# Performance work log

Measured on AMD Instinct MI355X. Metric: run time of the kernel, lower is better.

The kernel has to match this reference:

```python
import jax, jax.numpy as jnp
import numpy as np

K = 49        # k_neighbors
EPS = 1e-5    # BatchNorm2d eps


def setup_inputs() -> dict:
    key = jax.random.key(0)
    ks = jax.random.split(key, 2)
    B, C, M, O = 64, 64, 32, 128
    X = jax.random.normal(ks[0], (B, C, M, M), dtype=jnp.float32)
    # conv1x1 weight (kaiming fan_out) flattened to (O, C); bias init 0
    W = jax.random.normal(ks[1], (O, C), dtype=jnp.float32) * (2.0 / O) ** 0.5
    b = jnp.zeros((O,), jnp.float32)
    gamma = jnp.ones((O,), jnp.float32)
    beta = jnp.zeros((O,), jnp.float32)
    run_mean = jnp.zeros((O,), jnp.float32)
    run_var = jnp.ones((O,), jnp.float32)
    return dict(X=X, W=W, b=b, gamma=gamma, beta=beta,
                run_mean=run_mean, run_var=run_var)


def _knn_aggregate(x):
    """x: (N, C) node features -> D^{-1/2} A D^{-1/2} x for the kNN graph."""
    N = x.shape[0]
    sq = jnp.sum(x * x, axis=1)
    d2 = sq[:, None] + sq[None, :] - 2.0 * (x @ x.T)
    dist = jnp.sqrt(jnp.maximum(d2, 0.0))              # torch.cdist (p=2)
    i = jnp.arange(N)
    dist = dist.at[i, i].set(jnp.inf)                  # fill_diagonal_(inf)
    _, knn = jax.lax.top_k(-dist, K)                   # (N, K) nearest indices
    # topk indices are distinct -> every row degree == K, and the column
    # normalizer uses the col node's row degree (also K), so
    # D^{-1/2} A D^{-1/2} x == mean of gathered neighbors.
    nb = x[knn]                                        # (N, K, C) gather
    return nb.sum(axis=1) / K


def reference(X, W, b, gamma, beta, run_mean, run_var):
    B, C, M, _ = X.shape
    N = M * M
    x = X.reshape(B, C, N).transpose(0, 2, 1)          # (B, N, C) nodes
    Z = jax.vmap(_knn_aggregate)(x)                    # (B, N, C) sparse GCN agg
    # 1x1 conv over the (M, M) grid == per-node linear map
    Fg = jnp.einsum('oc,bnc->bon', W, Z) + b[None, :, None]   # (B, O, N)
    Fg = jax.nn.relu(Fg)
    # BatchNorm2d with running stats (eval mode); Dropout2d is identity in eval
    inv = jax.lax.rsqrt(run_var + EPS)
    Fg = gamma[None, :, None] * (Fg - run_mean[None, :, None]) * inv[None, :, None] + beta[None, :, None]
    return Fg.mean(axis=2)                             # AdaptiveAvgPool2d(1) -> (B, O)
```

## Files before the change

### kernel.cpp

```cpp
#include <hip/hip_runtime.h>
#include <stdint.h>

#define BATCH 64
#define CDIM  64
#define NPTS  1024
#define ODIM  128
#define KNN   49
#define KNNP  52
#define BNEPS 1e-5f
#define ZPAD  72

typedef __attribute__((ext_vector_type(8))) short bf16x8;
typedef __attribute__((ext_vector_type(4))) float f32x4;
typedef union { bf16x8 v; uint32_t d[4]; } bfu;

__device__ __forceinline__ int mbcnt64(unsigned long long m) {
    return __builtin_amdgcn_mbcnt_hi((uint32_t)(m >> 32),
           __builtin_amdgcn_mbcnt_lo((uint32_t)m, 0));
}

__device__ __forceinline__ void bf16_split(float x, uint32_t& h, uint32_t& l) {
    uint32_t u = __float_as_uint(x);
    h = (u + 0x7FFFu + ((u >> 16) & 1u)) >> 16;
    float hf = __uint_as_float(h << 16);
    uint32_t ul = __float_as_uint(x - hf);
    l = (ul + 0x7FFFu + ((ul >> 16) & 1u)) >> 16;
}

#define O_XF   0
#define SZ_XF  (BATCH*64*2*64*8*4)
#define O_SQ   (O_XF + SZ_XF)
#define SZ_SQ  (BATCH*NPTS*4)
#define O_KNN  (O_SQ + SZ_SQ)
#define SZ_KNN (BATCH*NPTS*KNNP*4)
#define O_XFT  (O_KNN + SZ_KNN)
#define SZ_XFT (BATCH*32*4*64*8*4)
#define WS_NEED ((size_t)(O_XFT + SZ_XFT))

__global__ void gcn_init(const float* __restrict__ gamma, const float* __restrict__ beta,
                         const float* __restrict__ rmean, const float* __restrict__ rvar,
                         float* __restrict__ out) {
    int i = blockIdx.x * 256 + threadIdx.x;
    if (i < BATCH * ODIM) {
        int o = i & (ODIM - 1);
        out[i] = beta[o] - gamma[o] * rmean[o] * rsqrtf(rvar[o] + BNEPS);
    }
}

__global__ __launch_bounds__(256) void k0_split(const float* __restrict__ X,
                                                uint32_t* __restrict__ XF,
                                                float* __restrict__ sq,
                                                uint32_t* __restrict__ XFT,
                                                const float* __restrict__ gamma,
                                                const float* __restrict__ beta,
                                                const float* __restrict__ rmean,
                                                const float* __restrict__ rvar,
                                                float* __restrict__ out) {
    if (blockIdx.x < 32) {
        int i = blockIdx.x * 256 + threadIdx.x;
        int o = i & (ODIM - 1);
        out[i] = beta[o] - gamma[o] * rmean[o] * rsqrtf(rvar[o] + BNEPS);
    }
    const int b    = blockIdx.x >> 4;
    const int g    = blockIdx.x & 15;
    const int wv   = threadIdx.x >> 6;
    const int t16  = g * 4 + wv;
    const int lane = threadIdx.x & 63;
    const int n    = t16 * 16 + (lane & 15);
    const int cg   = lane >> 4;
    const float* Xb = X + (size_t)b * CDIM * NPTS;
    float s = 0.f;
    for (int ks = 0; ks < 2; ks++) {
        uint32_t hi[4], lo[4];
#pragma unroll
        for (int dj = 0; dj < 4; dj++) {
            uint32_t hw[2], lw[2];
#pragma unroll
            for (int e = 0; e < 2; e++) {
                int c = ks * 32 + cg * 8 + dj * 2 + e;
                float x = Xb[(size_t)c * NPTS + n];
                s += x * x;
                bf16_split(x, hw[e], lw[e]);
            }
            hi[dj] = hw[0] | (hw[1] << 16);
            lo[dj] = lw[0] | (lw[1] << 16);
        }
        size_t entry = ((size_t)(b * 64 + t16) * 2 + ks) * 64 + lane;
        uint32_t* p = XF + entry * 8;
        *(uint4*)p       = make_uint4(hi[0], hi[1], hi[2], hi[3]);
        *(uint4*)(p + 4) = make_uint4(lo[0], lo[1], lo[2], lo[3]);
    }
    s += __shfl_xor(s, 16, 64);
    s += __shfl_xor(s, 32, 64);
    if (lane < 16) sq[b * NPTS + n] = s;

#pragma unroll
    for (int sx = 0; sx < 2; sx++) {
        int task = g * 8 + wv * 2 + sx;
        int kt = task >> 2, ct = task & 3;
        int c  = ct * 16 + (lane & 15);
        int n0 = kt * 32 + (lane >> 4) * 8;
        const float* xp = Xb + (size_t)c * NPTS + n0;
        uint32_t h[8], l[8];
#pragma unroll
        for (int j = 0; j < 8; j++) bf16_split(xp[j], h[j], l[j]);
        uint32_t* pp = XFT + ((((size_t)b * 32 + kt) * 4 + ct) * 64 + lane) * 8;
        *(uint4*)pp       = make_uint4(h[0] | (h[1] << 16), h[2] | (h[3] << 16),
                                       h[4] | (h[5] << 16), h[6] | (h[7] << 16));
        *(uint4*)(pp + 4) = make_uint4(l[0] | (l[1] << 16), l[2] | (l[3] << 16),
                                       l[4] | (l[5] << 16), l[6] | (l[7] << 16));
    }
}

__global__ __launch_bounds__(512, 6) void k1_gram_select(const uint32_t* __restrict__ XF,
                                                         const float* __restrict__ sq,
                                                         int* __restrict__ knn) {
    __shared__ uint32_t s_pk[8 * 1024];
    const int b    = blockIdx.x >> 6;
    const int rt   = blockIdx.x & 63;
    const int wave = threadIdx.x >> 6, lane = threadIdx.x & 63;
    const int q = lane >> 4, l15 = lane & 15;

    bf16x8 ahi[2], alo[2];
#pragma unroll
    for (int ks = 0; ks < 2; ks++) {
        const uint32_t* p = XF + (((size_t)(b * 64 + rt) * 2 + ks) * 64 + lane) * 8;
        ahi[ks] = *(const bf16x8*)p;
        alo[ks] = *(const bf16x8*)(p + 4);
    }
    const float* sqb = sq + b * NPTS;

#pragma unroll
    for (int tt = 0; tt < 8; tt++) {
        const int t16 = wave * 8 + tt;
        f32x4 acc = {0.f, 0.f, 0.f, 0.f};
#pragma unroll
        for (int ks = 0; ks < 2; ks++) {
            const uint32_t* p = XF + (((size_t)(b * 64 + t16) * 2 + ks) * 64 + lane) * 8;
            bf16x8 bhi = *(const bf16x8*)p;
            bf16x8 blo = *(const bf16x8*)(p + 4);
            acc = __builtin_amdgcn_mfma_f32_16x16x32_bf16(ahi[ks], bhi, acc, 0, 0, 0);
            acc = __builtin_amdgcn_mfma_f32_16x16x32_bf16(alo[ks], bhi, acc, 0, 0, 0);
            acc = __builtin_amdgcn_mfma_f32_16x16x32_bf16(ahi[ks], blo, acc, 0, 0, 0);
        }
        const int col  = t16 * 16 + l15;
        const float sqv = sqb[col];
        uint32_t k16[4];
#pragma unroll
        for (int i = 0; i < 4; i++) {
            int row = q * 4 + i;
            float d = fmaf(-2.f, acc[i], sqv);
            if (col == rt * 16 + row) d = __uint_as_float(0x7F800000u);
            uint32_t u = __float_as_uint(d);
            uint32_t key = ((int)u < 0) ? ~u : (u | 0x80000000u);
            k16[i] = key >> 16;
        }
        const int p0 = 2 * q, p1 = 2 * q + 1;
        s_pk[p0 * 1024 + (col ^ ((p0 & 3) << 3))] = k16[0] | (k16[1] << 16);
        s_pk[p1 * 1024 + (col ^ ((p1 & 3) << 3))] = k16[2] | (k16[3] << 16);
    }
    __syncthreads();

    uint32_t k0r[16], k1r[16];
    {
        const int sw = (wave & 3) << 3;
#pragma unroll
        for (int tt = 0; tt < 16; tt++) {
            uint32_t pk = s_pk[wave * 1024 + ((tt * 64 + lane) ^ sw)];
            k0r[tt] = pk & 0xFFFFu;
            k1r[tt] = pk >> 16;
        }
    }

    uint32_t lo0, hi0, lo1, hi1;
    {
        uint32_t lm0 = k0r[0], lm1 = k1r[0];
#pragma unroll
        for (int tt = 1; tt < 16; tt++) {
            lm0 = k0r[tt] < lm0 ? k0r[tt] : lm0;
            lm1 = k1r[tt] < lm1 ? k1r[tt] : lm1;
        }
        uint32_t g0 = lm0, m0 = lm0, g1 = lm1, m1 = lm1;
#pragma unroll
        for (int off = 1; off < 64; off <<= 1) {
            uint32_t a0 = (uint32_t)__shfl_xor((int)g0, off, 64);
            uint32_t b0 = (uint32_t)__shfl_xor((int)m0, off, 64);
            uint32_t a1 = (uint32_t)__shfl_xor((int)g1, off, 64);
            uint32_t b1 = (uint32_t)__shfl_xor((int)m1, off, 64);
            g0 = a0 < g0 ? a0 : g0;  m0 = b0 > m0 ? b0 : m0;
            g1 = a1 < g1 ? a1 : g1;  m1 = b1 > m1 ? b1 : m1;
        }
        lo0 = g0; hi0 = m0;
        lo1 = g1; hi1 = m1;
    }

    for (int it = 0; it < 16; it++) {
        bool a0 = lo0 < hi0, a1 = lo1 < hi1;
        if (!a0 && !a1) break;
        uint32_t mid0 = (lo0 + hi0) >> 1;
        uint32_t mid1 = (lo1 + hi1) >> 1;
        int cnt0 = 0, cnt1 = 0;
#pragma unroll
        for (int tt = 0; tt < 16; tt++) {
            cnt0 += __popcll(__ballot(k0r[tt] <= mid0));
            cnt1 += __popcll(__ballot(k1r[tt] <= mid1));
        }
        if (a0) { if (cnt0 >= KNN) hi0 = mid0; else lo0 = mid0 + 1; }
        if (a1) { if (cnt1 >= KNN) hi1 = mid1; else lo1 = mid1 + 1; }
    }

#pragma unroll
    for (int r = 0; r < 2; r++) {
        const int row = wave * 2 + r;
        const uint32_t vstar = r ? lo1 : lo0;
        const uint32_t* k = r ? k1r : k0r;
        int total_lt = 0;
#pragma unroll
        for (int tt = 0; tt < 16; tt++)
            total_lt += __popcll(__ballot(k[tt] < vstar));
        int base_lt = 0, base_eq = total_lt;
        int* kout = knn + ((size_t)b * NPTS + rt * 16 + row) * KNNP;
#pragma unroll
        for (int tt = 0; tt < 16; tt++) {
            bool islt = k[tt] < vstar;
            bool iseq = k[tt] == vstar;
            unsigned long long mlt = __ballot(islt);
            unsigned long long meq = __ballot(iseq);
            if (mlt | meq) {
                int pos = islt ? (base_lt + mbcnt64(mlt)) : (base_eq + mbcnt64(meq));
                if (islt || (iseq && pos < KNN)) kout[pos] = tt * 64 + lane;
            }
            base_lt += __popcll(mlt);
            base_eq += __popcll(meq);
        }
    }
}

__global__ __launch_bounds__(256) void k2_agg(const uint32_t* __restrict__ XFT,
                                              const int* __restrict__ knn,
                                              const float* __restrict__ W,
                                              const float* __restrict__ bias,
                                              const float* __restrict__ gamma,
                                              const float* __restrict__ rvar,
                                              float* __restrict__ out) {
    __shared__ uint32_t bm[128][33];
    __shared__ __align__(16) uint16_t ZFh[128 * ZPAD];
    __shared__ __align__(16) uint16_t ZFl[128 * ZPAD];
    __shared__ float red[512];
    const int b = blockIdx.x >> 3, nq = blockIdx.x & 7;
    const int t = threadIdx.x;
    const int wave = t >> 6, lane = t & 63;
    const int q = lane >> 4, l15 = lane & 15;

    {
        uint32_t* bf = &bm[0][0];
#pragma unroll
        for (int i = 0; i < 17; i++) {
            int idx = i * 256 + t;
            if (idx < 4224) bf[idx] = 0u;
        }
    }
    __syncthreads();
    {
        const int row = t >> 1, gg = t & 1;
        const int* kr = knn + ((size_t)b * NPTS + nq * 128 + row) * KNNP;
        int4 j[13];
#pragma unroll
        for (int c = 0; c < 13; c++) j[c] = *(const int4*)&kr[c * 4];
        if (gg == 0) {
#pragma unroll
            for (int c = 0; c < 6; c++) {
                int js[4] = {j[c].x, j[c].y, j[c].z, j[c].w};
#pragma unroll
                for (int e = 0; e < 4; e++)
                    atomicOr(&bm[row][js[e] >> 5], 1u << (js[e] & 31));
            }
        } else {
#pragma unroll
            for (int c = 6; c < 12; c++) {
                int js[4] = {j[c].x, j[c].y, j[c].z, j[c].w};
#pragma unroll
                for (int e = 0; e < 4; e++)
                    atomicOr(&bm[row][js[e] >> 5], 1u << (js[e] & 31));
            }
            atomicOr(&bm[row][j[12].x >> 5], 1u << (j[12].x & 31));
        }
    }
    __syncthreads();

    const int ct = wave;
    f32x4 acc[8];
#pragma unroll
    for (int mt = 0; mt < 8; mt++) acc[mt] = (f32x4){0.f, 0.f, 0.f, 0.f};
    for (int kt = 0; kt < 32; kt++) {
        const uint32_t* p = XFT + ((((size_t)b * 32 + kt) * 4 + ct) * 64 + lane) * 8;
        bf16x8 bhi = *(const bf16x8*)p;
        bf16x8 blo = *(const bf16x8*)(p + 4);
#pragma unroll
        for (int mt = 0; mt < 8; mt++) {
            uint32_t byte = (bm[mt * 16 + l15][kt] >> (q * 8)) & 0xFFu;
            bfu a;
            a.d[0] = ((byte & 1u)  ? 0x3F80u : 0u) | ((byte & 2u)   ? 0x3F800000u : 0u);
            a.d[1] = ((byte & 4u)  ? 0x3F80u : 0u) | ((byte & 8u)   ? 0x3F800000u : 0u);
            a.d[2] = ((byte & 16u) ? 0x3F80u : 0u) | ((byte & 32u)  ? 0x3F800000u : 0u);
            a.d[3] = ((byte & 64u) ? 0x3F80u : 0u) | ((byte & 128u) ? 0x3F800000u : 0u);
            acc[mt] = __builtin_amdgcn_mfma_f32_16x16x32_bf16(a.v, bhi, acc[mt], 0, 0, 0);
            acc[mt] = __builtin_amdgcn_mfma_f32_16x16x32_bf16(a.v, blo, acc[mt], 0, 0, 0);
        }
    }

#pragma unroll
    for (int mt = 0; mt < 8; mt++) {
#pragma unroll
        for (int reg = 0; reg < 4; reg++) {
            int r = mt * 16 + q * 4 + reg;
            int c = ct * 16 + l15;
            uint32_t h, l;
            bf16_split(acc[mt][reg], h, l);
            ZFh[r * ZPAD + c] = (uint16_t)h;
            ZFl[r * ZPAD + c] = (uint16_t)l;
        }
    }
    __syncthreads();

    bf16x8 zah[2][2], zal[2][2];
#pragma unroll
    for (int m2 = 0; m2 < 2; m2++) {
        const int m = (wave * 2 + m2) * 16 + l15;
#pragma unroll
        for (int kt = 0; kt < 2; kt++) {
            const int kb = kt * 32 + q * 8;
            zah[m2][kt] = *(const bf16x8*)&ZFh[m * ZPAD + kb];
            zal[m2][kt] = *(const bf16x8*)&ZFl[m * ZPAD + kb];
        }
    }
    const float inv49 = 1.f / KNN;
    float p[8];
#pragma unroll
    for (int nt = 0; nt < 8; nt++) {
        const int o = nt * 16 + l15;
        bfu wh[2], wl[2];
#pragma unroll
        for (int kt = 0; kt < 2; kt++) {
            const float* wp = W + (size_t)o * CDIM + kt * 32 + q * 8;
            float4 wa = *(const float4*)wp;
            float4 wb = *(const float4*)(wp + 4);
            float wv[8] = {wa.x, wa.y, wa.z, wa.w, wb.x, wb.y, wb.z, wb.w};
            uint32_t h[8], l[8];
#pragma unroll
            for (int e = 0; e < 8; e++) bf16_split(wv[e], h[e], l[e]);
#pragma unroll
            for (int dd = 0; dd < 4; dd++) {
                wh[kt].d[dd] = h[2 * dd] | (h[2 * dd + 1] << 16);
                wl[kt].d[dd] = l[2 * dd] | (l[2 * dd + 1] << 16);
            }
        }
        f32x4 acc0 = {0.f, 0.f, 0.f, 0.f};
        f32x4 acc1 = {0.f, 0.f, 0.f, 0.f};
#pragma unroll
        for (int kt = 0; kt < 2; kt++) {
            acc0 = __builtin_amdgcn_mfma_f32_16x16x32_bf16(zah[0][kt], wh[kt].v, acc0, 0, 0, 0);
            acc0 = __builtin_amdgcn_mfma_f32_16x16x32_bf16(zal[0][kt], wh[kt].v, acc0, 0, 0, 0);
            acc0 = __builtin_amdgcn_mfma_f32_16x16x32_bf16(zah[0][kt], wl[kt].v, acc0, 0, 0, 0);
            acc1 = __builtin_amdgcn_mfma_f32_16x16x32_bf16(zah[1][kt], wh[kt].v, acc1, 0, 0, 0);
            acc1 = __builtin_amdgcn_mfma_f32_16x16x32_bf16(zal[1][kt], wh[kt].v, acc1, 0, 0, 0);
            acc1 = __builtin_amdgcn_mfma_f32_16x16x32_bf16(zah[1][kt], wl[kt].v, acc1, 0, 0, 0);
        }
        const float bo = bias[o];
        float s = 0.f;
#pragma unroll
        for (int reg = 0; reg < 4; reg++) {
            s += fmaxf(fmaf(acc0[reg], inv49, bo), 0.f);
            s += fmaxf(fmaf(acc1[reg], inv49, bo), 0.f);
        }
        p[nt] = s;
    }
#pragma unroll
    for (int nt = 0; nt < 8; nt++) {
        p[nt] += __shfl_xor(p[nt], 16, 64);
        p[nt] += __shfl_xor(p[nt], 32, 64);
    }
    if (lane < 16) {
#pragma unroll
        for (int nt = 0; nt < 8; nt++)
            red[wave * 128 + nt * 16 + l15] = p[nt];
    }
    __syncthreads();
    if (t < 128) {
        float s = red[t] + red[128 + t] + red[256 + t] + red[384 + t];
        float scale = gamma[t] * rsqrtf(rvar[t] + BNEPS) * (1.f / NPTS);
        atomicAdd(&out[b * ODIM + t], s * scale);
    }
}

#define RTILE 8
#define APAD  1028
#define WPAD  132
#define POOLF (64 * WPAD)

__global__ __launch_bounds__(256) void gcn_main(
    const float* __restrict__ X, const float* __restrict__ W,
    const float* __restrict__ bias, const float* __restrict__ gamma,
    const float* __restrict__ rvar, float* __restrict__ out)
{
    __shared__ __align__(16) float s_pool[POOLF];
    __shared__ __align__(16) float s_fstage[4][APAD];
    __shared__ int   s_knn[RTILE][KNN];
    __shared__ float s_z[RTILE][CDIM];

    const int t = threadIdx.x;
    const int b = blockIdx.x >> 7;
    const int rtile = blockIdx.x & 127;
    const int r0 = rtile * RTILE;
    const float* Xb = X + (size_t)b * CDIM * NPTS;

    float acc[RTILE][4];
    float sqv[4];
#pragma unroll
    for (int r = 0; r < RTILE; r++)
#pragma unroll
        for (int u = 0; u < 4; u++) acc[r][u] = 0.f;
#pragma unroll
    for (int u = 0; u < 4; u++) sqv[u] = 0.f;

    for (int ch = 0; ch < 16; ch++) {
        const int c0 = ch * 4;
#pragma unroll
        for (int cc = 0; cc < 4; cc++) {
            float4 v = *(const float4*)(Xb + (size_t)(c0 + cc) * NPTS + 4 * t);
            *(float4*)&s_fstage[cc][4 * t] = v;
        }
        __syncthreads();
#pragma unroll
        for (int cc = 0; cc < 4; cc++) {
            float4 bv4 = *(const float4*)&s_fstage[cc][4 * t];
            float bv[4] = {bv4.x, bv4.y, bv4.z, bv4.w};
#pragma unroll
            for (int u = 0; u < 4; u++) sqv[u] += bv[u] * bv[u];
            const float* arow = Xb + (size_t)(c0 + cc) * NPTS + r0;
            float4 a0 = *(const float4*)(arow);
            float4 a1 = *(const float4*)(arow + 4);
            float av[8] = {a0.x, a0.y, a0.z, a0.w, a1.x, a1.y, a1.z, a1.w};
#pragma unroll
            for (int r = 0; r < RTILE; r++)
#pragma unroll
                for (int u = 0; u < 4; u++) acc[r][u] += av[r] * bv[u];
        }
        __syncthreads();
    }

    float* s_dist = s_pool;
#pragma unroll
    for (int r = 0; r < RTILE; r++) {
        const int rG = r0 + r;
        float d[4];
#pragma unroll
        for (int u = 0; u < 4; u++) {
            float dd = sqv[u] - 2.f * acc[r][u];
            d[u] = (4 * t + u == rG) ? __uint_as_float(0x7F800000u) : dd;
        }
        *(float4*)&s_dist[r * NPTS + 4 * t] = make_float4(d[0], d[1], d[2], d[3]);
    }
    __syncthreads();

    const int wave = t >> 6, lane = t & 63;
    const unsigned long long ltmask = (1ull << lane) - 1ull;
    for (int rr = 0; rr < 2; rr++) {
        const int row = wave * 2 + rr;
        unsigned key[16];
#pragma unroll
        for (int tt = 0; tt < 16; tt++) {
            unsigned u = __float_as_uint(s_dist[row * NPTS + tt * 64 + lane]);
            key[tt] = (u & 0x80000000u) ? ~u : (u | 0x80000000u);
        }
        unsigned lo = 0u, hi = 0xFFFFFFFFu;
        while (lo < hi) {
            unsigned mid = lo + ((hi - lo) >> 1);
            int cnt = 0;
#pragma unroll
            for (int tt = 0; tt < 16; tt++)
                cnt += __popcll(__ballot(key[tt] <= mid));
            if (cnt >= KNN) hi = mid; else lo = mid + 1;
        }
        const unsigned v49 = lo;
        int cntless = 0;
#pragma unroll
        for (int tt = 0; tt < 16; tt++)
            cntless += __popcll(__ballot(key[tt] < v49));
        const int need = KNN - cntless;
        int base = 0, eqtaken = 0;
#pragma unroll
        for (int tt = 0; tt < 16; tt++) {
            bool islt = key[tt] < v49;
            bool iseq = key[tt] == v49;
            unsigned long long meq = __ballot(iseq);
            int eqrank = eqtaken + __popcll(meq & ltmask);
            bool sel = islt || (iseq && (eqrank < need));
            unsigned long long msel = __ballot(sel);
            if (sel) {
                int pos = base + __popcll(msel & ltmask);
                s_knn[row][pos] = tt * 64 + lane;
            }
            base    += __popcll(msel);
            eqtaken += __popcll(meq);
        }
    }
    __syncthreads();

    float* astage = s_pool;
    float* s_redf = (float*)s_fstage;
    const int ar = t >> 5, acc8 = (t & 31) >> 2, ks = t & 3;
    for (int c0 = 0; c0 < CDIM; c0 += 8) {
#pragma unroll
        for (int qq = 0; qq < 8; qq++) {
            int if4 = qq * 256 + t;
            int cc = if4 >> 8, j4 = if4 & 255;
            float4 v = *(const float4*)(Xb + (size_t)(c0 + cc) * NPTS + 4 * j4);
            *(float4*)&astage[cc * APAD + 4 * j4] = v;
        }
        __syncthreads();
        float partial = 0.f;
        for (int k = ks; k < KNN; k += 4)
            partial += astage[acc8 * APAD + s_knn[ar][k]];
        s_redf[t] = partial;
        __syncthreads();
        if (t < 64) {
            int r = t >> 3, cc = t & 7;
            int bi = r * 32 + cc * 4;
            s_z[r][c0 + cc] = s_redf[bi] + s_redf[bi + 1] + s_redf[bi + 2] + s_redf[bi + 3];
        }
        __syncthreads();
    }

    float* wt = s_pool;
#pragma unroll 4
    for (int qq = 0; qq < 32; qq++) {
        int e = qq * 256 + t;
        int o = e >> 6, c = e & 63;
        wt[c * WPAD + o] = W[e];
    }
    __syncthreads();
    const int o = t & 127, rg = t >> 7;
    float facc[4] = {0.f, 0.f, 0.f, 0.f};
    for (int c = 0; c < CDIM; c += 4) {
        float w0 = wt[(c + 0) * WPAD + o], w1 = wt[(c + 1) * WPAD + o];
        float w2 = wt[(c + 2) * WPAD + o], w3 = wt[(c + 3) * WPAD + o];
#pragma unroll
        for (int qq = 0; qq < 4; qq++) {
            float4 zv = *(const float4*)&s_z[rg * 4 + qq][c];
            facc[qq] += w0 * zv.x + w1 * zv.y + w2 * zv.z + w3 * zv.w;
        }
    }
    const float bo = bias[o];
    float rsum = 0.f;
#pragma unroll
    for (int qq = 0; qq < 4; qq++) {
        float f = facc[qq] * (1.f / KNN) + bo;
        rsum += fmaxf(f, 0.f);
    }
    s_redf[t] = rsum;
    __syncthreads();
    if (t < 128) {
        float scale = gamma[t] * rsqrtf(rvar[t] + BNEPS) * (1.f / NPTS);
        atomicAdd(&out[b * ODIM + t], (s_redf[t] + s_redf[t + 128]) * scale);
    }
}

extern "C" void kernel_launch(void* const* d_in, const int* in_sizes, int n_in,
                              void* d_out, int out_size, void* d_ws, size_t ws_size,
                              hipStream_t stream) {
    const float* X     = (const float*)d_in[0];
    const float* W     = (const float*)d_in[1];
    const float* bias  = (const float*)d_in[2];
    const float* gamma = (const float*)d_in[3];
    const float* beta  = (const float*)d_in[4];
    const float* rmean = (const float*)d_in[5];
    const float* rvar  = (const float*)d_in[6];
    float* out = (float*)d_out;

    if (ws_size >= WS_NEED) {
        uint8_t* ws = (uint8_t*)d_ws;
        uint32_t* XF  = (uint32_t*)(ws + O_XF);
        float*    sqw = (float*)(ws + O_SQ);
        int*      knn = (int*)(ws + O_KNN);
        uint32_t* XFT = (uint32_t*)(ws + O_XFT);
        k0_split<<<BATCH * 16, 256, 0, stream>>>(X, XF, sqw, XFT,
                                                 gamma, beta, rmean, rvar, out);
        k1_gram_select<<<BATCH * 64, 512, 0, stream>>>(XF, sqw, knn);
        k2_agg<<<BATCH * 8, 256, 0, stream>>>(XFT, knn, W, bias, gamma, rvar, out);
    } else {
        gcn_init<<<(BATCH * ODIM + 255) / 256, 256, 0, stream>>>(gamma, beta, rmean, rvar, out);
        gcn_main<<<BATCH * (NPTS / RTILE), 256, 0, stream>>>(X, W, bias, gamma, rvar, out);
    }
}
```

Baseline: 242.8 us.

## Fuse kNN selection with neighbor aggregation and projection via shared-memory bitmasks

The selection kernel now writes each row's chosen neighbors as a bitmask into shared memory and directly performs the mask-times-features MFMA aggregation, the W projection, ReLU and pooled atomic accumulation. This removes the global kNN index buffer write/read and the separate aggregation kernel launch. W is pre-split into bf16 hi/lo fragments once in the split kernel. The cost is that every 16-row block re-streams the batch's full transposed feature matrix (XFT), so there is more L2 traffic, plus many more atomics to the output.

After: 245.3 us. About the same (+1.0%).

```diff
diff --git a/kernel.cpp b/kernel.cpp
--- a/kernel.cpp
+++ b/kernel.cpp
@@ -31,9 +31,11 @@
 #define SZ_XF  (BATCH*64*2*64*8*4)
 #define O_SQ   (O_XF + SZ_XF)
 #define SZ_SQ  (BATCH*NPTS*4)
-#define O_KNN  (O_SQ + SZ_SQ)
-#define SZ_KNN (BATCH*NPTS*KNNP*4)
-#define O_XFT  (O_KNN + SZ_KNN)
+#define O_WF   (O_SQ + SZ_SQ)
+#define SZ_WF  (2*16*64*16)
+#define O_PAD  (O_WF + SZ_WF)
+#define SZ_PAD (13631488 - SZ_WF)
+#define O_XFT  (O_PAD + SZ_PAD)
 #define SZ_XFT (BATCH*32*4*64*8*4)
 #define WS_NEED ((size_t)(O_XFT + SZ_XFT))
 
@@ -48,9 +50,12 @@
 }
 
 __global__ __launch_bounds__(256) void k0_split(const float* __restrict__ X,
+                                                const float* __restrict__ W,
                                                 uint32_t* __restrict__ XF,
                                                 float* __restrict__ sq,
                                                 uint32_t* __restrict__ XFT,
+                                                uint32_t* __restrict__ WFh,
+                                                uint32_t* __restrict__ WFl,
                                                 const float* __restrict__ gamma,
                                                 const float* __restrict__ beta,
                                                 const float* __restrict__ rmean,
@@ -60,6 +65,20 @@
         int i = blockIdx.x * 256 + threadIdx.x;
         int o = i & (ODIM - 1);
         out[i] = beta[o] - gamma[o] * rmean[o] * rsqrtf(rvar[o] + BNEPS);
+    } else if (blockIdx.x < 36) {
+        int item = (blockIdx.x - 32) * 256 + threadIdx.x;
+        int e = item >> 6, ln = item & 63;
+        int nt = e >> 1, kt = e & 1;
+        int o = nt * 16 + (ln & 15);
+        int kc = kt * 32 + (ln >> 4) * 8;
+        const float* wp = W + (size_t)o * CDIM + kc;
+        uint32_t h[8], l[8];
+#pragma unroll
+        for (int jj = 0; jj < 8; jj++) bf16_split(wp[jj], h[jj], l[jj]);
+        *(uint4*)&WFh[item * 4] = make_uint4(h[0] | (h[1] << 16), h[2] | (h[3] << 16),
+                                             h[4] | (h[5] << 16), h[6] | (h[7] << 16));
+        *(uint4*)&WFl[item * 4] = make_uint4(l[0] | (l[1] << 16), l[2] | (l[3] << 16),
+                                             l[4] | (l[5] << 16), l[6] | (l[7] << 16));
     }
     const int b    = blockIdx.x >> 4;
     const int g    = blockIdx.x & 15;
@@ -112,10 +131,17 @@
     }
 }
 
-__global__ __launch_bounds__(512, 6) void k1_gram_select(const uint32_t* __restrict__ XF,
-                                                         const float* __restrict__ sq,
-                                                         int* __restrict__ knn) {
+__global__ __launch_bounds__(512, 6) void k1_fused(const uint32_t* __restrict__ XF,
+                                                   const float* __restrict__ sq,
+                                                   const uint32_t* __restrict__ XFT,
+                                                   const uint32_t* __restrict__ WFh,
+                                                   const uint32_t* __restrict__ WFl,
+                                                   const float* __restrict__ bias,
+                                                   const float* __restrict__ gamma,
+                                                   const float* __restrict__ rvar,
+                                                   float* __restrict__ out) {
     __shared__ uint32_t s_pk[8 * 1024];
+    __shared__ uint32_t bm[16][33];
     const int b    = blockIdx.x >> 6;
     const int rt   = blockIdx.x & 63;
     const int wave = threadIdx.x >> 6, lane = threadIdx.x & 63;
@@ -218,178 +244,95 @@
 #pragma unroll
         for (int tt = 0; tt < 16; tt++)
             total_lt += __popcll(__ballot(k[tt] < vstar));
-        int base_lt = 0, base_eq = total_lt;
-        int* kout = knn + ((size_t)b * NPTS + rt * 16 + row) * KNNP;
+        int base_eq = total_lt;
 #pragma unroll
         for (int tt = 0; tt < 16; tt++) {
             bool islt = k[tt] < vstar;
             bool iseq = k[tt] == vstar;
-            unsigned long long mlt = __ballot(islt);
             unsigned long long meq = __ballot(iseq);
-            if (mlt | meq) {
-                int pos = islt ? (base_lt + mbcnt64(mlt)) : (base_eq + mbcnt64(meq));
-                if (islt || (iseq && pos < KNN)) kout[pos] = tt * 64 + lane;
-            }
-            base_lt += __popcll(mlt);
+            int pos = base_eq + mbcnt64(meq);
+            bool sel = islt || (iseq && pos < KNN);
+            unsigned long long msel = __ballot(sel);
+            if (lane < 2)
+                bm[row][tt * 2 + lane] = lane ? (uint32_t)(msel >> 32) : (uint32_t)msel;
             base_eq += __popcll(meq);
         }
     }
-}
-
-__global__ __launch_bounds__(256) void k2_agg(const uint32_t* __restrict__ XFT,
-                                              const int* __restrict__ knn,
-                                              const float* __restrict__ W,
-                                              const float* __restrict__ bias,
-                                              const float* __restrict__ gamma,
-                                              const float* __restrict__ rvar,
-                                              float* __restrict__ out) {
-    __shared__ uint32_t bm[128][33];
-    __shared__ __align__(16) uint16_t ZFh[128 * ZPAD];
-    __shared__ __align__(16) uint16_t ZFl[128 * ZPAD];
-    __shared__ float red[512];
-    const int b = blockIdx.x >> 3, nq = blockIdx.x & 7;
-    const int t = threadIdx.x;
-    const int wave = t >> 6, lane = t & 63;
-    const int q = lane >> 4, l15 = lane & 15;
-
+    __syncthreads();
+
+    float* redp = (float*)s_pk;
+    uint16_t* ZFh = (uint16_t*)(s_pk + 2048);
+    uint16_t* ZFl = ZFh + 16 * ZPAD;
     {
-        uint32_t* bf = &bm[0][0];
-#pragma unroll
-        for (int i = 0; i < 17; i++) {
-            int idx = i * 256 + t;
-            if (idx < 4224) bf[idx] = 0u;
-        }
-    }
-    __syncthreads();
-    {
-        const int row = t >> 1, gg = t & 1;
-        const int* kr = knn + ((size_t)b * NPTS + nq * 128 + row) * KNNP;
-        int4 j[13];
-#pragma unroll
-        for (int c = 0; c < 13; c++) j[c] = *(const int4*)&kr[c * 4];
-        if (gg == 0) {
-#pragma unroll
-            for (int c = 0; c < 6; c++) {
-                int js[4] = {j[c].x, j[c].y, j[c].z, j[c].w};
-#pragma unroll
-                for (int e = 0; e < 4; e++)
-                    atomicOr(&bm[row][js[e] >> 5], 1u << (js[e] & 31));
-            }
-        } else {
-#pragma unroll
-            for (int c = 6; c < 12; c++) {
-                int js[4] = {j[c].x, j[c].y, j[c].z, j[c].w};
-#pragma unroll
-                for (int e = 0; e < 4; e++)
-                    atomicOr(&bm[row][js[e] >> 5], 1u << (js[e] & 31));
-            }
-            atomicOr(&bm[row][j[12].x >> 5], 1u << (j[12].x & 31));
-        }
-    }
-    __syncthreads();
-
-    const int ct = wave;
-    f32x4 acc[8];
-#pragma unroll
-    for (int mt = 0; mt < 8; mt++) acc[mt] = (f32x4){0.f, 0.f, 0.f, 0.f};
-    for (int kt = 0; kt < 32; kt++) {
-        const uint32_t* p = XFT + ((((size_t)b * 32 + kt) * 4 + ct) * 64 + lane) * 8;
-        bf16x8 bhi = *(const bf16x8*)p;
-        bf16x8 blo = *(const bf16x8*)(p + 4);
-#pragma unroll
-        for (int mt = 0; mt < 8; mt++) {
-            uint32_t byte = (bm[mt * 16 + l15][kt] >> (q * 8)) & 0xFFu;
+        const int ct = wave >> 1, kh = wave & 1;
+        f32x4 za = {0.f, 0.f, 0.f, 0.f};
+#pragma unroll
+        for (int ki = 0; ki < 16; ki++) {
+            const int kt = kh * 16 + ki;
+            const uint32_t* p = XFT + ((((size_t)b * 32 + kt) * 4 + ct) * 64 + lane) * 8;
+            bf16x8 bhi = *(const bf16x8*)p;
+            bf16x8 blo = *(const bf16x8*)(p + 4);
+            uint32_t byte = (bm[l15][kt] >> (q * 8)) & 0xFFu;
             bfu a;
             a.d[0] = ((byte & 1u)  ? 0x3F80u : 0u) | ((byte & 2u)   ? 0x3F800000u : 0u);
             a.d[1] = ((byte & 4u)  ? 0x3F80u : 0u) | ((byte & 8u)   ? 0x3F800000u : 0u);
             a.d[2] = ((byte & 16u) ? 0x3F80u : 0u) | ((byte & 32u)  ? 0x3F800000u : 0u);
             a.d[3] = ((byte & 64u) ? 0x3F80u : 0u) | ((byte & 128u) ? 0x3F800000u : 0u);
-            acc[mt] = __builtin_amdgcn_mfma_f32_16x16x32_bf16(a.v, bhi, acc[mt], 0, 0, 0);
-            acc[mt] = __builtin_amdgcn_mfma_f32_16x16x32_bf16(a.v, blo, acc[mt], 0, 0, 0);
-        }
-    }
-
-#pragma unroll
-    for (int mt = 0; mt < 8; mt++) {
-#pragma unroll
-        for (int reg = 0; reg < 4; reg++) {
-            int r = mt * 16 + q * 4 + reg;
-            int c = ct * 16 + l15;
+            za = __builtin_amdgcn_mfma_f32_16x16x32_bf16(a.v, bhi, za, 0, 0, 0);
+            za = __builtin_amdgcn_mfma_f32_16x16x32_bf16(a.v, blo, za, 0, 0, 0);
+        }
+        *(f32x4*)&redp[(wave * 64 + lane) * 4] = za;
+    }
+    __syncthreads();
+    if (wave < 4) {
+        const int ctw = wave;
+        f32x4 za = *(const f32x4*)&redp[((2 * ctw) * 64 + lane) * 4];
+        f32x4 zb = *(const f32x4*)&redp[((2 * ctw + 1) * 64 + lane) * 4];
+#pragma unroll
+        for (int i = 0; i < 4; i++) {
             uint32_t h, l;
-            bf16_split(acc[mt][reg], h, l);
-            ZFh[r * ZPAD + c] = (uint16_t)h;
-            ZFl[r * ZPAD + c] = (uint16_t)l;
-        }
-    }
-    __syncthreads();
-
-    bf16x8 zah[2][2], zal[2][2];
-#pragma unroll
-    for (int m2 = 0; m2 < 2; m2++) {
-        const int m = (wave * 2 + m2) * 16 + l15;
+            bf16_split(za[i] + zb[i], h, l);
+            const int rr = q * 4 + i, cc = ctw * 16 + l15;
+            ZFh[rr * ZPAD + cc] = (uint16_t)h;
+            ZFl[rr * ZPAD + cc] = (uint16_t)l;
+        }
+    }
+    __syncthreads();
+
+    {
+        const int nt = wave, o = nt * 16 + l15;
+        bf16x8 zah[2], zal[2];
 #pragma unroll
         for (int kt = 0; kt < 2; kt++) {
             const int kb = kt * 32 + q * 8;
-            zah[m2][kt] = *(const bf16x8*)&ZFh[m * ZPAD + kb];
-            zal[m2][kt] = *(const bf16x8*)&ZFl[m * ZPAD + kb];
-        }
-    }
-    const float inv49 = 1.f / KNN;
-    float p[8];
-#pragma unroll
-    for (int nt = 0; nt < 8; nt++) {
-        const int o = nt * 16 + l15;
+            zah[kt] = *(const bf16x8*)&ZFh[l15 * ZPAD + kb];
+            zal[kt] = *(const bf16x8*)&ZFl[l15 * ZPAD + kb];
+        }
         bfu wh[2], wl[2];
 #pragma unroll
         for (int kt = 0; kt < 2; kt++) {
-            const float* wp = W + (size_t)o * CDIM + kt * 32 + q * 8;
-            float4 wa = *(const float4*)wp;
-            float4 wb = *(const float4*)(wp + 4);
-            float wv[8] = {wa.x, wa.y, wa.z, wa.w, wb.x, wb.y, wb.z, wb.w};
-            uint32_t h[8], l[8];
-#pragma unroll
-            for (int e = 0; e < 8; e++) bf16_split(wv[e], h[e], l[e]);
-#pragma unroll
-            for (int dd = 0; dd < 4; dd++) {
-                wh[kt].d[dd] = h[2 * dd] | (h[2 * dd + 1] << 16);
-                wl[kt].d[dd] = l[2 * dd] | (l[2 * dd + 1] << 16);
-            }
-        }
-        f32x4 acc0 = {0.f, 0.f, 0.f, 0.f};
-        f32x4 acc1 = {0.f, 0.f, 0.f, 0.f};
+            const int item = (nt * 2 + kt) * 64 + lane;
+            *(uint4*)wh[kt].d = *(const uint4*)&WFh[item * 4];
+            *(uint4*)wl[kt].d = *(const uint4*)&WFl[item * 4];
+        }
+        f32x4 accw = {0.f, 0.f, 0.f, 0.f};
 #pragma unroll
         for (int kt = 0; kt < 2; kt++) {
-            acc0 = __builtin_amdgcn_mfma_f32_16x16x32_bf16(zah[0][kt], wh[kt].v, acc0, 0, 0, 0);
-            acc0 = __builtin_amdgcn_mfma_f32_16x16x32_bf16(zal[0][kt], wh[kt].v, acc0, 0, 0, 0);
-            acc0 = __builtin_amdgcn_mfma_f32_16x16x32_bf16(zah[0][kt], wl[kt].v, acc0, 0, 0, 0);
-            acc1 = __builtin_amdgcn_mfma_f32_16x16x32_bf16(zah[1][kt], wh[kt].v, acc1, 0, 0, 0);
-            acc1 = __builtin_amdgcn_mfma_f32_16x16x32_bf16(zal[1][kt], wh[kt].v, acc1, 0, 0, 0);
-            acc1 = __builtin_amdgcn_mfma_f32_16x16x32_bf16(zah[1][kt], wl[kt].v, acc1, 0, 0, 0);
+            accw = __builtin_amdgcn_mfma_f32_16x16x32_bf16(zah[kt], wh[kt].v, accw, 0, 0, 0);
+            accw = __builtin_amdgcn_mfma_f32_16x16x32_bf16(zal[kt], wh[kt].v, accw, 0, 0, 0);
+            accw = __builtin_amdgcn_mfma_f32_16x16x32_bf16(zah[kt], wl[kt].v, accw, 0, 0, 0);
         }
         const float bo = bias[o];
         float s = 0.f;
 #pragma unroll
-        for (int reg = 0; reg < 4; reg++) {
-            s += fmaxf(fmaf(acc0[reg], inv49, bo), 0.f);
-            s += fmaxf(fmaf(acc1[reg], inv49, bo), 0.f);
-        }
-        p[nt] = s;
-    }
-#pragma unroll
-    for (int nt = 0; nt < 8; nt++) {
-        p[nt] += __shfl_xor(p[nt], 16, 64);
-        p[nt] += __shfl_xor(p[nt], 32, 64);
-    }
-    if (lane < 16) {
-#pragma unroll
-        for (int nt = 0; nt < 8; nt++)
-            red[wave * 128 + nt * 16 + l15] = p[nt];
-    }
-    __syncthreads();
-    if (t < 128) {
-        float s = red[t] + red[128 + t] + red[256 + t] + red[384 + t];
-        float scale = gamma[t] * rsqrtf(rvar[t] + BNEPS) * (1.f / NPTS);
-        atomicAdd(&out[b * ODIM + t], s * scale);
+        for (int reg = 0; reg < 4; reg++)
+            s += fmaxf(fmaf(accw[reg], 1.f / KNN, bo), 0.f);
+        s += __shfl_xor(s, 16, 64);
+        s += __shfl_xor(s, 32, 64);
+        if (lane < 16) {
+            float scale = gamma[o] * rsqrtf(rvar[o] + BNEPS) * (1.f / NPTS);
+            atomicAdd(&out[b * ODIM + o], s * scale);
+        }
     }
 }
 
@@ -582,12 +525,13 @@
         uint8_t* ws = (uint8_t*)d_ws;
         uint32_t* XF  = (uint32_t*)(ws + O_XF);
         float*    sqw = (float*)(ws + O_SQ);
-        int*      knn = (int*)(ws + O_KNN);
+        uint32_t* WFh = (uint32_t*)(ws + O_WF);
+        uint32_t* WFl = WFh + 16 * 64 * 4;
         uint32_t* XFT = (uint32_t*)(ws + O_XFT);
-        k0_split<<<BATCH * 16, 256, 0, stream>>>(X, XF, sqw, XFT,
+        k0_split<<<BATCH * 16, 256, 0, stream>>>(X, W, XF, sqw, XFT, WFh, WFl,
                                                  gamma, beta, rmean, rvar, out);
-        k1_gram_select<<<BATCH * 64, 512, 0, stream>>>(XF, sqw, knn);
-        k2_agg<<<BATCH * 8, 256, 0, stream>>>(XFT, knn, W, bias, gamma, rvar, out);
+        k1_fused<<<BATCH * 64, 512, 0, stream>>>(XF, sqw, XFT, WFh, WFl,
+                                                 bias, gamma, rvar, out);
     } else {
         gcn_init<<<(BATCH * ODIM + 255) / 256, 256, 0, stream>>>(gamma, beta, rmean, rvar, out);
         gcn_main<<<BATCH * (NPTS / RTILE), 256, 0, stream>>>(X, W, bias, gamma, rvar, out);
```

## Emit kNN selection as bitmask in select kernel; pre-split W once

Applied to the files above, without the earlier changes.

The select kernel now writes each row's neighbor set directly as a 1024-bit bitmask, built from wave ballots and staged through shared memory, instead of a padded list of 52 indices. The aggregation kernel then copies the bitmask straight into shared memory, which removes its zero-fill pass and its shared-memory atomicOr scatter. The kNN intermediate shrinks from 208 to 128 bytes per row, and the per-row index scatter becomes coalesced vector stores. Separately, W is split into bf16 hi/lo MFMA fragments once in k0 instead of in every aggregation block, at the cost of an extra workspace buffer and a dependency on k0.

New measurement: 230.9 us (median of 2 runs). 4.9% less time.

```diff
diff --git a/kernel.cpp b/kernel.cpp
--- a/kernel.cpp
+++ b/kernel.cpp
@@ -31,9 +31,11 @@
 #define SZ_XF  (BATCH*64*2*64*8*4)
 #define O_SQ   (O_XF + SZ_XF)
 #define SZ_SQ  (BATCH*NPTS*4)
-#define O_KNN  (O_SQ + SZ_SQ)
-#define SZ_KNN (BATCH*NPTS*KNNP*4)
-#define O_XFT  (O_KNN + SZ_KNN)
+#define O_WF   (O_SQ + SZ_SQ)
+#define SZ_WF  (2*16*64*16)
+#define O_BM   (O_WF + SZ_WF)
+#define SZ_BM  (BATCH*NPTS*32*4)
+#define O_XFT  (O_BM + SZ_BM)
 #define SZ_XFT (BATCH*32*4*64*8*4)
 #define WS_NEED ((size_t)(O_XFT + SZ_XFT))
 
@@ -48,9 +50,12 @@
 }
 
 __global__ __launch_bounds__(256) void k0_split(const float* __restrict__ X,
+                                                const float* __restrict__ W,
                                                 uint32_t* __restrict__ XF,
                                                 float* __restrict__ sq,
                                                 uint32_t* __restrict__ XFT,
+                                                uint32_t* __restrict__ WFh,
+                                                uint32_t* __restrict__ WFl,
                                                 const float* __restrict__ gamma,
                                                 const float* __restrict__ beta,
                                                 const float* __restrict__ rmean,
@@ -60,6 +65,20 @@
         int i = blockIdx.x * 256 + threadIdx.x;
         int o = i & (ODIM - 1);
         out[i] = beta[o] - gamma[o] * rmean[o] * rsqrtf(rvar[o] + BNEPS);
+    } else if (blockIdx.x < 36) {
+        int item = (blockIdx.x - 32) * 256 + threadIdx.x;
+        int e = item >> 6, ln = item & 63;
+        int nt = e >> 1, kt = e & 1;
+        int o = nt * 16 + (ln & 15);
+        int kc = kt * 32 + (ln >> 4) * 8;
+        const float* wp = W + (size_t)o * CDIM + kc;
+        uint32_t h[8], l[8];
+#pragma unroll
+        for (int jj = 0; jj < 8; jj++) bf16_split(wp[jj], h[jj], l[jj]);
+        *(uint4*)&WFh[item * 4] = make_uint4(h[0] | (h[1] << 16), h[2] | (h[3] << 16),
+                                             h[4] | (h[5] << 16), h[6] | (h[7] << 16));
+        *(uint4*)&WFl[item * 4] = make_uint4(l[0] | (l[1] << 16), l[2] | (l[3] << 16),
+                                             l[4] | (l[5] << 16), l[6] | (l[7] << 16));
     }
     const int b    = blockIdx.x >> 4;
     const int g    = blockIdx.x & 15;
@@ -114,8 +133,9 @@
 
 __global__ __launch_bounds__(512, 6) void k1_gram_select(const uint32_t* __restrict__ XF,
                                                          const float* __restrict__ sq,
-                                                         int* __restrict__ knn) {
+                                                         uint32_t* __restrict__ BM) {
     __shared__ uint32_t s_pk[8 * 1024];
+    __shared__ uint32_t s_bm[16][32];
     const int b    = blockIdx.x >> 6;
     const int rt   = blockIdx.x & 63;
     const int wave = threadIdx.x >> 6, lane = threadIdx.x & 63;
@@ -218,32 +238,36 @@
 #pragma unroll
         for (int tt = 0; tt < 16; tt++)
             total_lt += __popcll(__ballot(k[tt] < vstar));
-        int base_lt = 0, base_eq = total_lt;
-        int* kout = knn + ((size_t)b * NPTS + rt * 16 + row) * KNNP;
+        int base_eq = total_lt;
 #pragma unroll
         for (int tt = 0; tt < 16; tt++) {
             bool islt = k[tt] < vstar;
             bool iseq = k[tt] == vstar;
-            unsigned long long mlt = __ballot(islt);
             unsigned long long meq = __ballot(iseq);
-            if (mlt | meq) {
-                int pos = islt ? (base_lt + mbcnt64(mlt)) : (base_eq + mbcnt64(meq));
-                if (islt || (iseq && pos < KNN)) kout[pos] = tt * 64 + lane;
-            }
-            base_lt += __popcll(mlt);
+            int pos = base_eq + mbcnt64(meq);
+            bool sel = islt || (iseq && pos < KNN);
+            unsigned long long msel = __ballot(sel);
+            if (lane < 2)
+                s_bm[row][tt * 2 + lane] = lane ? (uint32_t)(msel >> 32) : (uint32_t)msel;
             base_eq += __popcll(meq);
         }
     }
+    __syncthreads();
+    if (threadIdx.x < 128) {
+        uint32_t* dst = BM + ((size_t)(b * NPTS + rt * 16) * 32);
+        *(uint4*)&dst[threadIdx.x * 4] = *(const uint4*)&((const uint32_t*)s_bm)[threadIdx.x * 4];
+    }
 }
 
 __global__ __launch_bounds__(256) void k2_agg(const uint32_t* __restrict__ XFT,
-                                              const int* __restrict__ knn,
-                                              const float* __restrict__ W,
+                                              const uint32_t* __restrict__ BM,
+                                              const uint32_t* __restrict__ WFh,
+                                              const uint32_t* __restrict__ WFl,
                                               const float* __restrict__ bias,
                                               const float* __restrict__ gamma,
                                               const float* __restrict__ rvar,
                                               float* __restrict__ out) {
-    __shared__ uint32_t bm[128][33];
+    __shared__ uint32_t bmp[128 * 33];
     __shared__ __align__(16) uint16_t ZFh[128 * ZPAD];
     __shared__ __align__(16) uint16_t ZFl[128 * ZPAD];
     __shared__ float red[512];
@@ -253,37 +277,12 @@
     const int q = lane >> 4, l15 = lane & 15;
 
     {
-        uint32_t* bf = &bm[0][0];
-#pragma unroll
-        for (int i = 0; i < 17; i++) {
-            int idx = i * 256 + t;
-            if (idx < 4224) bf[idx] = 0u;
-        }
-    }
-    __syncthreads();
-    {
-        const int row = t >> 1, gg = t & 1;
-        const int* kr = knn + ((size_t)b * NPTS + nq * 128 + row) * KNNP;
-        int4 j[13];
-#pragma unroll
-        for (int c = 0; c < 13; c++) j[c] = *(const int4*)&kr[c * 4];
-        if (gg == 0) {
-#pragma unroll
-            for (int c = 0; c < 6; c++) {
-                int js[4] = {j[c].x, j[c].y, j[c].z, j[c].w};
-#pragma unroll
-                for (int e = 0; e < 4; e++)
-                    atomicOr(&bm[row][js[e] >> 5], 1u << (js[e] & 31));
-            }
-        } else {
-#pragma unroll
-            for (int c = 6; c < 12; c++) {
-                int js[4] = {j[c].x, j[c].y, j[c].z, j[c].w};
-#pragma unroll
-                for (int e = 0; e < 4; e++)
-                    atomicOr(&bm[row][js[e] >> 5], 1u << (js[e] & 31));
-            }
-            atomicOr(&bm[row][j[12].x >> 5], 1u << (j[12].x & 31));
+        const uint32_t* src = BM + ((size_t)(b * NPTS + nq * 128) * 32);
+#pragma unroll
+        for (int kk = 0; kk < 16; kk++) {
+            int idx = kk * 256 + t;
+            uint32_t v = src[idx];
+            bmp[(idx >> 5) * 33 + (idx & 31)] = v;
         }
     }
     __syncthreads();
@@ -298,7 +297,7 @@
         bf16x8 blo = *(const bf16x8*)(p + 4);
 #pragma unroll
         for (int mt = 0; mt < 8; mt++) {
-            uint32_t byte = (bm[mt * 16 + l15][kt] >> (q * 8)) & 0xFFu;
+            uint32_t byte = (bmp[(mt * 16 + l15) * 33 + kt] >> (q * 8)) & 0xFFu;
             bfu a;
             a.d[0] = ((byte & 1u)  ? 0x3F80u : 0u) | ((byte & 2u)   ? 0x3F800000u : 0u);
             a.d[1] = ((byte & 4u)  ? 0x3F80u : 0u) | ((byte & 8u)   ? 0x3F800000u : 0u);
@@ -342,18 +341,9 @@
         bfu wh[2], wl[2];
 #pragma unroll
         for (int kt = 0; kt < 2; kt++) {
-            const float* wp = W + (size_t)o * CDIM + kt * 32 + q * 8;
-            float4 wa = *(const float4*)wp;
-            float4 wb = *(const float4*)(wp + 4);
-            float wv[8] = {wa.x, wa.y, wa.z, wa.w, wb.x, wb.y, wb.z, wb.w};
-            uint32_t h[8], l[8];
-#pragma unroll
-            for (int e = 0; e < 8; e++) bf16_split(wv[e], h[e], l[e]);
-#pragma unroll
-            for (int dd = 0; dd < 4; dd++) {
-                wh[kt].d[dd] = h[2 * dd] | (h[2 * dd + 1] << 16);
-                wl[kt].d[dd] = l[2 * dd] | (l[2 * dd + 1] << 16);
-            }
+            const int item = (nt * 2 + kt) * 64 + lane;
+            *(uint4*)wh[kt].d = *(const uint4*)&WFh[item * 4];
+            *(uint4*)wl[kt].d = *(const uint4*)&WFl[item * 4];
         }
         f32x4 acc0 = {0.f, 0.f, 0.f, 0.f};
         f32x4 acc1 = {0.f, 0.f, 0.f, 0.f};
@@ -582,12 +572,14 @@
         uint8_t* ws = (uint8_t*)d_ws;
         uint32_t* XF  = (uint32_t*)(ws + O_XF);
         float*    sqw = (float*)(ws + O_SQ);
-        int*      knn = (int*)(ws + O_KNN);
+        uint32_t* WFh = (uint32_t*)(ws + O_WF);
+        uint32_t* WFl = WFh + 16 * 64 * 4;
+        uint32_t* BM  = (uint32_t*)(ws + O_BM);
         uint32_t* XFT = (uint32_t*)(ws + O_XFT);
-        k0_split<<<BATCH * 16, 256, 0, stream>>>(X, XF, sqw, XFT,
+        k0_split<<<BATCH * 16, 256, 0, stream>>>(X, W, XF, sqw, XFT, WFh, WFl,
                                                  gamma, beta, rmean, rvar, out);
-        k1_gram_select<<<BATCH * 64, 512, 0, stream>>>(XF, sqw, knn);
-        k2_agg<<<BATCH * 8, 256, 0, stream>>>(XFT, knn, W, bias, gamma, rvar, out);
+        k1_gram_select<<<BATCH * 64, 512, 0, stream>>>(XF, sqw, BM);
+        k2_agg<<<BATCH * 8, 256, 0, stream>>>(XFT, BM, WFh, WFl, bias, gamma, rvar, out);
     } else {
         gcn_init<<<(BATCH * ODIM + 255) / 256, 256, 0, stream>>>(gamma, beta, rmean, rvar, out);
         gcn_main<<<BATCH * (NPTS / RTILE), 256, 0, stream>>>(X, W, bias, gamma, rvar, out);
```
